# Optimization experiments

Hardware: AMD Instinct MI355X
Metric: run time of the kernel (lower is better)

Reference implementation:

```python
import jax, jax.numpy as jnp
from jax import lax
import numpy as np

V, H, L = 32000, 512, 256   # vocab, hidden_dim, latent_dim
B, TE, TD = 16, 512, 256    # batch, enc max len, dec max len


def setup_inputs() -> dict:
    key = jax.random.key(0)
    ks = jax.random.split(key, 20)
    s = 0.05
    inp = {}
    inp['emb'] = jax.random.normal(ks[0], (V, H), jnp.float32) * s
    # GRU params, PyTorch layout: W_ih [3H_out, D_in], gate order r,z,n
    inp['enc_Wih'] = jax.random.normal(ks[1], (3 * H, H), jnp.float32) * s
    inp['enc_Whh'] = jax.random.normal(ks[2], (3 * H, H), jnp.float32) * s
    inp['enc_bih'] = jnp.zeros((3 * H,), jnp.float32)
    inp['enc_bhh'] = jnp.zeros((3 * H,), jnp.float32)
    inp['dec_Wih'] = jax.random.normal(ks[3], (3 * L, H), jnp.float32) * s
    inp['dec_Whh'] = jax.random.normal(ks[4], (3 * L, L), jnp.float32) * s
    inp['dec_bih'] = jnp.zeros((3 * L,), jnp.float32)
    inp['dec_bhh'] = jnp.zeros((3 * L,), jnp.float32)
    inp['W_mu'] = jax.random.normal(ks[5], (L, 2 * H), jnp.float32) * s
    inp['b_mu'] = jnp.zeros((L,), jnp.float32)
    inp['W_ls'] = jax.random.normal(ks[6], (L, 2 * H), jnp.float32) * s
    inp['b_ls'] = jnp.zeros((L,), jnp.float32)
    inp['W_fc'] = jax.random.normal(ks[7], (V, L), jnp.float32) * s
    inp['b_fc'] = jnp.zeros((V,), jnp.float32)
    inp['noise'] = jax.random.normal(ks[8], (B, L), jnp.float32)  # reparam eps
    inp['enc_ids'] = jax.random.randint(ks[9], (B, TE), 0, V)
    inp['enc_len'] = jax.random.randint(ks[10], (B,), 1, TE + 1)
    inp['dec_ids'] = jax.random.randint(ks[11], (B, TD), 0, V)
    inp['dec_len'] = jax.random.randint(ks[12], (B,), 1, TD + 1)
    return inp


def gru(x, lengths, h0, Wih, Whh, bih, bhh):
    # x: [B,T,D], h0: [B,Hout]. Emulates packed GRU: state frozen and output
    # zeroed past each sample's length (pad_packed_sequence semantics).
    T = x.shape[1]
    Hout = h0.shape[-1]
    xT = jnp.swapaxes(x, 0, 1)                              # [T,B,D]
    valid = jnp.arange(T)[:, None] < lengths[None, :]       # [T,B]

    def step(h, inp):
        x_t, v = inp
        gx = x_t @ Wih.T + bih                              # [B,3Hout]
        gh = h @ Whh.T + bhh
        r = jax.nn.sigmoid(gx[:, :Hout] + gh[:, :Hout])
        z = jax.nn.sigmoid(gx[:, Hout:2 * Hout] + gh[:, Hout:2 * Hout])
        n = jnp.tanh(gx[:, 2 * Hout:] + r * gh[:, 2 * Hout:])
        h_new = (1.0 - z) * n + z * h
        h_keep = jnp.where(v[:, None], h_new, h)
        out = jnp.where(v[:, None], h_new, 0.0)
        return h_keep, out

    h_last, outs = lax.scan(step, h0, (xT, valid))
    return jnp.swapaxes(outs, 0, 1), h_last                 # [B,T,Hout], [B,Hout]


def masked_softmax(scores, mask):
    s = jnp.where(mask, scores, -jnp.inf)
    a = jax.nn.softmax(s, axis=-1)
    return jnp.where(mask, a, 0.0)


def reference(emb, enc_Wih, enc_Whh, enc_bih, enc_bhh,
              dec_Wih, dec_Whh, dec_bih, dec_bhh,
              W_mu, b_mu, W_ls, b_ls, W_fc, b_fc, noise,
              enc_ids, enc_len, dec_ids, dec_len):
    # ---- encode ----
    x_enc = emb[enc_ids]                                    # [B,TE,H]
    h0 = jnp.zeros((x_enc.shape[0], H), x_enc.dtype)
    out, last_state = gru(x_enc, enc_len, h0, enc_Wih, enc_Whh, enc_bih, enc_bhh)
    mask = jnp.arange(out.shape[1])[None, :] < enc_len[:, None]   # [B,TE]
    # batched masked attention pooling (replaces per-sample _return_weight loop)
    first_state = out[:, 0, :]                              # out[0] always valid
    alpha_fw = masked_softmax(jnp.einsum('btd,bd->bt', out, last_state), mask)
    alpha_bw = masked_softmax(jnp.einsum('btd,bd->bt', out, first_state), mask)
    alpha = 0.5 * (alpha_fw + alpha_bw)
    semantic = jnp.einsum('bt,btd->bd', alpha, out)
    h_enc = jnp.concatenate([last_state, semantic], axis=1)  # [B,2H]
    # ---- sample latent ----
    mu = h_enc @ W_mu.T + b_mu
    sigma = jnp.exp(h_enc @ W_ls.T + b_ls)
    z = mu + sigma * noise
    # ---- decode ----
    x_dec = emb[dec_ids]                                    # [B,TD,H]
    dec_out, _ = gru(x_dec, dec_len, z, dec_Wih, dec_Whh, dec_bih, dec_bhh)
    logits = dec_out @ W_fc.T + b_fc                        # [B,TD,V]
    dec_max_len = jnp.max(dec_len)
    return logits, dec_max_len, mu, sigma
```

## Files before the change

### kernel.cpp

```cpp
#include <hip/hip_runtime.h>
#include <hip/hip_bf16.h>
#include <stdint.h>

#define B 16
#define H 512
#define L 256
#define TE 512
#define TD 256
#define NV 32000

typedef __attribute__((ext_vector_type(8))) __bf16 bf16x8;
typedef __attribute__((ext_vector_type(4))) float f32x4;
typedef __attribute__((ext_vector_type(8))) unsigned short u16x8;
typedef __attribute__((ext_vector_type(4))) unsigned short u16x4;
typedef unsigned short u16;
typedef unsigned long long u64;

__device__ __forceinline__ u16 f2bf(float f) {
  unsigned u = __float_as_uint(f);
  u += 0x7fffu + ((u >> 16) & 1u);
  return (u16)(u >> 16);
}
__device__ __forceinline__ float fast_sigmoid(float x) {
  return __builtin_amdgcn_rcpf(1.f + __expf(-x));
}
__device__ __forceinline__ float fast_tanh(float x) {
  float e = __expf(2.f * x);
  return 1.f - 2.f * __builtin_amdgcn_rcpf(e + 1.f);
}

__device__ __forceinline__ u16x8 pack8(float4 a, float4 c) {
  u16x8 r;
  r[0] = f2bf(a.x); r[1] = f2bf(a.y); r[2] = f2bf(a.z); r[3] = f2bf(a.w);
  r[4] = f2bf(c.x); r[5] = f2bf(c.y); r[6] = f2bf(c.z); r[7] = f2bf(c.w);
  return r;
}

__global__ __launch_bounds__(256) void k_f2bf(const float* __restrict__ in,
                                              u16* __restrict__ outp, long n) {
  long i = ((long)blockIdx.x * 256 + threadIdx.x) * 8;
  if (i + 8 > n) return;
  float4 a = *(const float4*)&in[i];
  float4 c = *(const float4*)&in[i + 4];
  *(u16x8*)&outp[i] = pack8(a, c);
}

__global__ __launch_bounds__(256) void k_gather(const float* __restrict__ emb,
                                                const int* __restrict__ ids,
                                                u16* __restrict__ X, int rows) {
  int gid = blockIdx.x * 256 + threadIdx.x;
  int m = gid >> 6, seg = gid & 63;
  if (m >= rows) return;
  long src = (long)ids[m] * H + seg * 8;
  float4 a = *(const float4*)&emb[src];
  float4 c = *(const float4*)&emb[src + 4];
  *(u16x8*)&X[(long)m * H + seg * 8] = pack8(a, c);
}

__global__ __launch_bounds__(256) void k_gemm_bt(const u16* __restrict__ A,
                                                 const u16* __restrict__ Bw,
                                                 const float* __restrict__ bias,
                                                 float* __restrict__ C,
                                                 int M, int N, int K) {
  constexpr int LDSK = 72;
  __shared__ u16 Al[128 * LDSK];
  __shared__ u16 Bl[128 * LDSK];
  const int tid = threadIdx.x;
  const int lane = tid & 63;
  const int wave = tid >> 6;
  const int wr = (wave >> 1) * 64, wc = (wave & 1) * 64;
  const long tM = (long)blockIdx.y * 128, tN = (long)blockIdx.x * 128;
  const int r32 = tid >> 3;
  const int c8 = (tid & 7) * 8;
  const u16* Ag = A + (tM + r32) * (long)K + c8;
  const u16* Bg = Bw + (tN + r32) * (long)K + c8;
  const int fr = lane & 15;
  const int fq = lane >> 4;
  f32x4 acc[4][4] = {};

  for (int kb = 0; kb < K; kb += 64) {
    u16x8 ta0 = *(const u16x8*)(Ag + kb);
    u16x8 ta1 = *(const u16x8*)(Ag + 32 * (long)K + kb);
    u16x8 ta2 = *(const u16x8*)(Ag + 64 * (long)K + kb);
    u16x8 ta3 = *(const u16x8*)(Ag + 96 * (long)K + kb);
    u16x8 tb0 = *(const u16x8*)(Bg + kb);
    u16x8 tb1 = *(const u16x8*)(Bg + 32 * (long)K + kb);
    u16x8 tb2 = *(const u16x8*)(Bg + 64 * (long)K + kb);
    u16x8 tb3 = *(const u16x8*)(Bg + 96 * (long)K + kb);
    __syncthreads();
    *(u16x8*)&Al[(r32 +  0) * LDSK + c8] = ta0;
    *(u16x8*)&Al[(r32 + 32) * LDSK + c8] = ta1;
    *(u16x8*)&Al[(r32 + 64) * LDSK + c8] = ta2;
    *(u16x8*)&Al[(r32 + 96) * LDSK + c8] = ta3;
    *(u16x8*)&Bl[(r32 +  0) * LDSK + c8] = tb0;
    *(u16x8*)&Bl[(r32 + 32) * LDSK + c8] = tb1;
    *(u16x8*)&Bl[(r32 + 64) * LDSK + c8] = tb2;
    *(u16x8*)&Bl[(r32 + 96) * LDSK + c8] = tb3;
    __syncthreads();
#pragma unroll
    for (int ks = 0; ks < 2; ks++) {
      const int kcol = ks * 32 + fq * 8;
      bf16x8 av[4], bv[4];
#pragma unroll
      for (int mi = 0; mi < 4; mi++)
        av[mi] = __builtin_bit_cast(bf16x8, *(const u16x8*)&Al[(wr + mi * 16 + fr) * LDSK + kcol]);
#pragma unroll
      for (int ni = 0; ni < 4; ni++)
        bv[ni] = __builtin_bit_cast(bf16x8, *(const u16x8*)&Bl[(wc + ni * 16 + fr) * LDSK + kcol]);
#pragma unroll
      for (int mi = 0; mi < 4; mi++)
#pragma unroll
        for (int ni = 0; ni < 4; ni++)
          acc[mi][ni] = __builtin_amdgcn_mfma_f32_16x16x32_bf16(av[mi], bv[ni], acc[mi][ni], 0, 0, 0);
    }
  }
#pragma unroll
  for (int mi = 0; mi < 4; mi++) {
    long row = tM + wr + mi * 16 + fq * 4;
#pragma unroll
    for (int ni = 0; ni < 4; ni++) {
      long col = tN + wc + ni * 16 + fr;
      float bs = bias[col];
#pragma unroll
      for (int r = 0; r < 4; r++)
        C[(row + r) * (long)N + col] = acc[mi][ni][r] + bs;
    }
  }
}

template <bool ENC, int HD, int T, int UPW>
__global__ __launch_bounds__(256) void k_gru7(const float* __restrict__ GX,
                                              const float* __restrict__ Whh,
                                              const float* __restrict__ bhh,
                                              const int* __restrict__ lens,
                                              u64* __restrict__ Hbuf,
                                              const float* __restrict__ h0f,
                                              float* __restrict__ out_f32,
                                              u16* __restrict__ out_bf,
                                              float* __restrict__ hlast) {
  constexpr int G2 = UPW / 16;
  constexpr int ROWS = 3 * UPW;
  constexpr int LDH = HD + 8;
  constexpr int WPB = HD / 2;
  constexpr int NWORD = 16 * WPB;
  constexpr int PW = NWORD / 256;
  __shared__ u16 w_lds[ROWS][LDH];
  __shared__ u16 h_lds[16][LDH];

  const int tid = threadIdx.x;
  const int u0 = blockIdx.x * UPW;
  const int lane = tid & 63, wv = tid >> 6;
  const int fr = lane & 15, fq = lane >> 4;
  const bool cw = wv < G2;
  const int u = u0 + wv * 16 + fr;

  for (int i = tid; i < ROWS * HD / 4; i += 256) {
    int rr = i / (HD / 4), c = (i % (HD / 4)) * 4;
    int tt = rr >> 4, fr_ = rr & 15;
    int grow = (tt % 3) * HD + u0 + (tt / 3) * 16 + fr_;
    float4 v = *(const float4*)&Whh[(long)grow * HD + c];
    u16x4 p; p[0] = f2bf(v.x); p[1] = f2bf(v.y); p[2] = f2bf(v.z); p[3] = f2bf(v.w);
    *(u16x4*)&w_lds[rr][c] = p;
  }
  int tmax = 1;
#pragma unroll
  for (int i = 0; i < 16; i++) tmax = max(tmax, lens[i]);

  float bh[3], hold[4];
  int len4[4];
#pragma unroll
  for (int g = 0; g < 3; g++) bh[g] = cw ? bhh[g * HD + u] : 0.f;
#pragma unroll
  for (int r = 0; r < 4; r++) {
    len4[r] = cw ? lens[fq * 4 + r] : 0;
    hold[r] = (ENC || !cw) ? 0.f : h0f[(fq * 4 + r) * HD + u];
  }
  __syncthreads();

  for (int t = 0; ; t++) {
    const u64* Hc = Hbuf + (size_t)(t & 1) * NWORD;
    u64* Hn = Hbuf + (size_t)((t + 1) & 1) * NWORD;
    float gxr[3][4];
    if (cw) {
#pragma unroll
      for (int g = 0; g < 3; g++)
#pragma unroll
        for (int r = 0; r < 4; r++)
          gxr[g][r] = GX[((size_t)(fq * 4 + r) * T + t) * 3 * HD + g * HD + u];
    }
    const unsigned want = (unsigned)t;
    u64 vv[PW];
#pragma unroll
    for (int i = 0; i < PW; i++)
      vv[i] = __hip_atomic_load(&Hc[i * 256 + tid], __ATOMIC_RELAXED, __HIP_MEMORY_SCOPE_AGENT);
    for (;;) {
      bool ok = true;
#pragma unroll
      for (int i = 0; i < PW; i++) ok &= ((unsigned)(vv[i] >> 32) == want);
      if (ok) break;
#pragma unroll
      for (int i = 0; i < PW; i++)
        if ((unsigned)(vv[i] >> 32) != want)
          vv[i] = __hip_atomic_load(&Hc[i * 256 + tid], __ATOMIC_RELAXED, __HIP_MEMORY_SCOPE_AGENT);
    }
#pragma unroll
    for (int i = 0; i < PW; i++) {
      int w = i * 256 + tid;
      *(unsigned*)&h_lds[w / WPB][(w % WPB) * 2] = (unsigned)vv[i];
    }
    __syncthreads();
    if (cw) {
      f32x4 accg[3] = {};
#pragma unroll
      for (int kk = 0; kk < HD / 32; kk++) {
        int kc = kk * 32 + fq * 8;
        bf16x8 av = __builtin_bit_cast(bf16x8, *(const u16x8*)&h_lds[fr][kc]);
#pragma unroll
        for (int g = 0; g < 3; g++) {
          bf16x8 bv = __builtin_bit_cast(bf16x8,
              *(const u16x8*)&w_lds[(wv * 3 + g) * 16 + fr][kc]);
          accg[g] = __builtin_amdgcn_mfma_f32_16x16x32_bf16(av, bv, accg[g], 0, 0, 0);
        }
      }
#pragma unroll
      for (int r = 0; r < 4; r++) {
        const int bb = fq * 4 + r;
        const bool val = t < len4[r];
        float rr_ = fast_sigmoid(accg[0][r] + bh[0] + gxr[0][r]);
        float zz  = fast_sigmoid(accg[1][r] + bh[1] + gxr[1][r]);
        float nn  = fast_tanh(gxr[2][r] + rr_ * (accg[2][r] + bh[2]));
        float hnew = (1.f - zz) * nn + zz * hold[r];
        float hk = val ? hnew : hold[r];
        hold[r] = hk;
        float sh = __shfl_xor(hk, 1);
        if (!(fr & 1)) {
          u64 pw = ((u64)(unsigned)(t + 1) << 32) |
                   ((unsigned)f2bf(sh) << 16) | f2bf(hk);
          __hip_atomic_store(&Hn[(size_t)bb * WPB + ((unsigned)u >> 1)], pw,
                             __ATOMIC_RELAXED, __HIP_MEMORY_SCOPE_AGENT);
          if constexpr (ENC) {
            float2 o = val ? make_float2(hk, sh) : make_float2(0.f, 0.f);
            *(float2*)&out_f32[((size_t)bb * T + t) * HD + u] = o;
          } else {
            unsigned ow = val ? (((unsigned)f2bf(sh) << 16) | f2bf(hk)) : 0u;
            *(unsigned*)&out_bf[((size_t)bb * T + t) * HD + u] = ow;
          }
        }
      }
    }
    __syncthreads();
    if (t + 1 >= tmax) break;
  }

  if (cw) {
    if constexpr (ENC) {
#pragma unroll
      for (int r = 0; r < 4; r++) hlast[(fq * 4 + r) * HD + u] = hold[r];
    }
  }
  if constexpr (ENC) {
    float4 z4 = make_float4(0.f, 0.f, 0.f, 0.f);
    for (int bb = 0; bb < 16; bb++)
      for (int x = tid; x < (T - tmax) * HD / 4; x += 256) {
        int t2 = tmax + (x * 4) / HD, c = (x * 4) % HD;
        *(float4*)&out_f32[((size_t)bb * T + t2) * HD + c] = z4;
      }
  } else {
    u16x8 z8 = {};
    for (int bb = 0; bb < 16; bb++)
      for (int x = tid; x < (T - tmax) * HD / 8; x += 256) {
        int t2 = tmax + (x * 8) / HD, c = (x * 8) % HD;
        *(u16x8*)&out_bf[((size_t)bb * T + t2) * HD + c] = z8;
      }
  }
}

__global__ __launch_bounds__(256) void k_middle(const float* __restrict__ out_enc,
                                                const float* __restrict__ hlast,
                                                const int* __restrict__ enc_len,
                                                const float* __restrict__ W_mu,
                                                const float* __restrict__ b_mu,
                                                const float* __restrict__ W_ls,
                                                const float* __restrict__ b_ls,
                                                const float* __restrict__ noise,
                                                const int* __restrict__ dec_len,
                                                float* __restrict__ out_tail,
                                                float* __restrict__ zf,
                                                u64* __restrict__ hbw) {
  const int b = blockIdx.x, tid = threadIdx.x;
  __shared__ float last[H], first[H], sfw[TE], sbw[TE], alpha[TE], sem[H];
  __shared__ float redA[256], redB[256];
  __shared__ u16 zbf[L];
  const int len = enc_len[b];
  for (int i = tid; i < H; i += 256) {
    last[i] = hlast[b * H + i];
    first[i] = out_enc[((size_t)b * TE) * H + i];
  }
  __syncthreads();
  for (int t = tid; t < TE; t += 256) {
    float afw = 0.f, abw = 0.f;
    if (t < len) {
      const float4* op = (const float4*)&out_enc[((size_t)b * TE + t) * H];
      for (int i = 0; i < H / 4; i++) {
        float4 o = op[i];
        float4 l = *(const float4*)&last[i * 4];
        float4 f = *(const float4*)&first[i * 4];
        afw += o.x * l.x + o.y * l.y + o.z * l.z + o.w * l.w;
        abw += o.x * f.x + o.y * f.y + o.z * f.z + o.w * f.w;
      }
    }
    sfw[t] = afw; sbw[t] = abw;
  }
  __syncthreads();
  float mfw = -3e38f, mbw = -3e38f;
  for (int t = tid; t < len; t += 256) { mfw = fmaxf(mfw, sfw[t]); mbw = fmaxf(mbw, sbw[t]); }
  redA[tid] = mfw; redB[tid] = mbw; __syncthreads();
  for (int s = 128; s > 0; s >>= 1) {
    if (tid < s) { redA[tid] = fmaxf(redA[tid], redA[tid + s]); redB[tid] = fmaxf(redB[tid], redB[tid + s]); }
    __syncthreads();
  }
  const float Mfw = redA[0], Mbw = redB[0];
  __syncthreads();
  float tfw = 0.f, tbw = 0.f;
  for (int t = tid; t < len; t += 256) {
    float e1 = expf(sfw[t] - Mfw); sfw[t] = e1; tfw += e1;
    float e2 = expf(sbw[t] - Mbw); sbw[t] = e2; tbw += e2;
  }
  redA[tid] = tfw; redB[tid] = tbw; __syncthreads();
  for (int s = 128; s > 0; s >>= 1) {
    if (tid < s) { redA[tid] += redA[tid + s]; redB[tid] += redB[tid + s]; }
    __syncthreads();
  }
  const float ifw = 0.5f / redA[0], ibw = 0.5f / redB[0];
  __syncthreads();
  for (int t = tid; t < TE; t += 256) alpha[t] = (t < len) ? (sfw[t] * ifw + sbw[t] * ibw) : 0.f;
  __syncthreads();
  for (int d = tid; d < H; d += 256) {
    float s = 0.f;
    for (int t = 0; t < len; t++) s += alpha[t] * out_enc[((size_t)b * TE + t) * H + d];
    sem[d] = s;
  }
  __syncthreads();
  {
    const int j = tid;
    const float4* wm = (const float4*)&W_mu[(size_t)j * 2 * H];
    const float4* wl = (const float4*)&W_ls[(size_t)j * 2 * H];
    float am = 0.f, al = 0.f;
    for (int i = 0; i < H / 4; i++) {
      float4 hh = *(const float4*)&last[i * 4];
      float4 w1 = wm[i]; am += hh.x * w1.x + hh.y * w1.y + hh.z * w1.z + hh.w * w1.w;
      float4 w2 = wl[i]; al += hh.x * w2.x + hh.y * w2.y + hh.z * w2.z + hh.w * w2.w;
    }
    for (int i = 0; i < H / 4; i++) {
      float4 hh = *(const float4*)&sem[i * 4];
      float4 w1 = wm[H / 4 + i]; am += hh.x * w1.x + hh.y * w1.y + hh.z * w1.z + hh.w * w1.w;
      float4 w2 = wl[H / 4 + i]; al += hh.x * w2.x + hh.y * w2.y + hh.z * w2.z + hh.w * w2.w;
    }
    float muv = am + b_mu[j];
    float sgv = expf(al + b_ls[j]);
    float zv = muv + sgv * noise[b * L + j];
    out_tail[131072001ul + (size_t)b * L + j] = muv;
    out_tail[131076097ul + (size_t)b * L + j] = sgv;
    zf[b * L + j] = zv;
    zbf[j] = f2bf(zv);
  }
  __syncthreads();
  if (tid < L / 2) {
    u64 pw = ((unsigned)zbf[2 * tid + 1] << 16) | (u64)zbf[2 * tid];
    __hip_atomic_store(&hbw[b * (L / 2) + tid], pw,
                       __ATOMIC_RELAXED, __HIP_MEMORY_SCOPE_AGENT);
  }
  if (b == 0 && tid == 0) {
    int m = 0;
    for (int i = 0; i < B; i++) m = max(m, dec_len[i]);
    out_tail[131072000ul] = (float)m;
  }
}

extern "C" void kernel_launch(void* const* d_in, const int* in_sizes, int n_in,
                              void* d_out, int out_size, void* d_ws, size_t ws_size,
                              hipStream_t stream) {
  const float* emb     = (const float*)d_in[0];
  const float* eWih    = (const float*)d_in[1];
  const float* eWhh    = (const float*)d_in[2];
  const float* ebih    = (const float*)d_in[3];
  const float* ebhh    = (const float*)d_in[4];
  const float* dWih    = (const float*)d_in[5];
  const float* dWhh    = (const float*)d_in[6];
  const float* dbih    = (const float*)d_in[7];
  const float* dbhh    = (const float*)d_in[8];
  const float* W_mu    = (const float*)d_in[9];
  const float* b_mu    = (const float*)d_in[10];
  const float* W_ls    = (const float*)d_in[11];
  const float* b_ls    = (const float*)d_in[12];
  const float* W_fc    = (const float*)d_in[13];
  const float* b_fc    = (const float*)d_in[14];
  const float* noise   = (const float*)d_in[15];
  const int*   enc_ids = (const int*)d_in[16];
  const int*   enc_len = (const int*)d_in[17];
  const int*   dec_ids = (const int*)d_in[18];
  const int*   dec_len = (const int*)d_in[19];
  float* out = (float*)d_out;
  char* ws = (char*)d_ws;

  u16*   eWih_bf  = (u16*)(ws + 0);
  u16*   dWih_bf  = (u16*)(ws + 1572864);
  u16*   Wfc_bf   = (u16*)(ws + 2359296);
  u64*   Hbuf_enc = (u64*)(ws + 18743296);
  float* hlast    = (float*)(ws + 18808832);
  u64*   Hbuf_dec = (u64*)(ws + 18841600);
  u16*   dec_out  = (u16*)(ws + 18874368);
  float* zf       = (float*)(ws + 20971520);

  char* ob = (char*)d_out;
  u16*   Xenc_bf = (u16*)(ob + 0);
  u16*   Xdec_bf = (u16*)(ob + 8388608);
  float* GXE     = (float*)(ob + 12582912);
  float* GXD     = (float*)(ob + 62914560);
  float* out_enc = (float*)(ob + 75497472);

  hipMemsetAsync(Hbuf_enc, 0, 65536, stream);
  hipMemsetAsync(Hbuf_dec, 0, 32768, stream);

  k_f2bf<<<384, 256, 0, stream>>>(eWih, eWih_bf, 786432);
  k_f2bf<<<192, 256, 0, stream>>>(dWih, dWih_bf, 393216);
  k_f2bf<<<4000, 256, 0, stream>>>(W_fc, Wfc_bf, 8192000);
  k_gather<<<2048, 256, 0, stream>>>(emb, enc_ids, Xenc_bf, B * TE);
  k_gather<<<1024, 256, 0, stream>>>(emb, dec_ids, Xdec_bf, B * TD);

  k_gemm_bt<<<dim3(12, 64), 256, 0, stream>>>(Xenc_bf, eWih_bf, ebih, GXE, B * TE, 3 * H, H);
  k_gemm_bt<<<dim3(6, 32), 256, 0, stream>>>(Xdec_bf, dWih_bf, dbih, GXD, B * TD, 3 * L, H);

  k_gru7<true, H, TE, 32><<<16, 256, 0, stream>>>(GXE, eWhh, ebhh, enc_len, Hbuf_enc,
                                                  nullptr, out_enc, nullptr, hlast);

  k_middle<<<B, 256, 0, stream>>>(out_enc, hlast, enc_len, W_mu, b_mu, W_ls, b_ls,
                                  noise, dec_len, out, zf, Hbuf_dec);

  k_gru7<false, L, TD, 64><<<4, 256, 0, stream>>>(GXD, dWhh, dbhh, dec_len, Hbuf_dec,
                                                  zf, nullptr, dec_out, nullptr);

  k_gemm_bt<<<dim3(250, 32), 256, 0, stream>>>(dec_out, Wfc_bf, b_fc, out, B * TD, NV, L);
}
```

Before: 2.411 ms.

## Specialize GRU warps: compute waves poll state, helper waves prefetch GX and write outputs

The recurrent GRU kernel now splits each block into two compute waves that spin on the shared hidden state and run the MFMA step, plus two helper waves. The helper waves prefetch the next timestep's input-gate activations into double-buffered LDS and write the previous step's outputs from LDS with coalesced vector stores. This takes global GX loads and scattered output stores off the serial critical path. The decoder now uses 32 units per block with 8 blocks instead of 64 units with 4, which spreads the recurrence over more CUs but means more blocks polling each step.

```diff
diff --git a/kernel.cpp b/kernel.cpp
--- a/kernel.cpp
+++ b/kernel.cpp
@@ -128,8 +128,8 @@
   }
 }
 
-template <bool ENC, int HD, int T, int UPW>
-__global__ __launch_bounds__(256) void k_gru7(const float* __restrict__ GX,
+template <bool ENC, int HD, int T>
+__global__ __launch_bounds__(256) void k_gru8(const float* __restrict__ GX,
                                               const float* __restrict__ Whh,
                                               const float* __restrict__ bhh,
                                               const int* __restrict__ lens,
@@ -138,20 +138,23 @@
                                               float* __restrict__ out_f32,
                                               u16* __restrict__ out_bf,
                                               float* __restrict__ hlast) {
-  constexpr int G2 = UPW / 16;
+  constexpr int UPW = 32;
   constexpr int ROWS = 3 * UPW;
   constexpr int LDH = HD + 8;
   constexpr int WPB = HD / 2;
   constexpr int NWORD = 16 * WPB;
-  constexpr int PW = NWORD / 256;
+  constexpr int PW = NWORD / 128;
   __shared__ u16 w_lds[ROWS][LDH];
   __shared__ u16 h_lds[16][LDH];
+  __shared__ float gx_lds[2][3][16][33];
+  __shared__ float out_lds[2][16][33];
 
   const int tid = threadIdx.x;
   const int u0 = blockIdx.x * UPW;
   const int lane = tid & 63, wv = tid >> 6;
   const int fr = lane & 15, fq = lane >> 4;
-  const bool cw = wv < G2;
+  const bool cw = wv < 2;
+  const int ct = tid & 127;
   const int u = u0 + wv * 16 + fr;
 
   for (int i = tid; i < ROWS * HD / 4; i += 256) {
@@ -175,38 +178,67 @@
     len4[r] = cw ? lens[fq * 4 + r] : 0;
     hold[r] = (ENC || !cw) ? 0.f : h0f[(fq * 4 + r) * HD + u];
   }
+  if (!cw) {
+    const int b = ct >> 3, c0 = (ct & 7) * 4;
+#pragma unroll
+    for (int g = 0; g < 3; g++) {
+      float4 v = *(const float4*)&GX[((size_t)b * T) * 3 * HD + g * HD + u0 + c0];
+      gx_lds[0][g][b][c0 + 0] = v.x; gx_lds[0][g][b][c0 + 1] = v.y;
+      gx_lds[0][g][b][c0 + 2] = v.z; gx_lds[0][g][b][c0 + 3] = v.w;
+    }
+  }
   __syncthreads();
 
   for (int t = 0; ; t++) {
-    const u64* Hc = Hbuf + (size_t)(t & 1) * NWORD;
-    u64* Hn = Hbuf + (size_t)((t + 1) & 1) * NWORD;
-    float gxr[3][4];
+    const int cb_ = t & 1, nb_ = (t + 1) & 1;
     if (cw) {
-#pragma unroll
-      for (int g = 0; g < 3; g++)
-#pragma unroll
-        for (int r = 0; r < 4; r++)
-          gxr[g][r] = GX[((size_t)(fq * 4 + r) * T + t) * 3 * HD + g * HD + u];
-    }
-    const unsigned want = (unsigned)t;
-    u64 vv[PW];
-#pragma unroll
-    for (int i = 0; i < PW; i++)
-      vv[i] = __hip_atomic_load(&Hc[i * 256 + tid], __ATOMIC_RELAXED, __HIP_MEMORY_SCOPE_AGENT);
-    for (;;) {
-      bool ok = true;
-#pragma unroll
-      for (int i = 0; i < PW; i++) ok &= ((unsigned)(vv[i] >> 32) == want);
-      if (ok) break;
+      const u64* Hc = Hbuf + (size_t)cb_ * NWORD;
+      const unsigned want = (unsigned)t;
+      u64 vv[PW];
 #pragma unroll
       for (int i = 0; i < PW; i++)
-        if ((unsigned)(vv[i] >> 32) != want)
-          vv[i] = __hip_atomic_load(&Hc[i * 256 + tid], __ATOMIC_RELAXED, __HIP_MEMORY_SCOPE_AGENT);
-    }
-#pragma unroll
-    for (int i = 0; i < PW; i++) {
-      int w = i * 256 + tid;
-      *(unsigned*)&h_lds[w / WPB][(w % WPB) * 2] = (unsigned)vv[i];
+        vv[i] = __hip_atomic_load(&Hc[i * 128 + ct], __ATOMIC_RELAXED, __HIP_MEMORY_SCOPE_AGENT);
+      for (;;) {
+        bool ok = true;
+#pragma unroll
+        for (int i = 0; i < PW; i++) ok &= ((unsigned)(vv[i] >> 32) == want);
+        if (ok) break;
+#pragma unroll
+        for (int i = 0; i < PW; i++)
+          if ((unsigned)(vv[i] >> 32) != want)
+            vv[i] = __hip_atomic_load(&Hc[i * 128 + ct], __ATOMIC_RELAXED, __HIP_MEMORY_SCOPE_AGENT);
+      }
+#pragma unroll
+      for (int i = 0; i < PW; i++) {
+        int w = i * 128 + ct;
+        *(unsigned*)&h_lds[w / WPB][(w % WPB) * 2] = (unsigned)vv[i];
+      }
+    } else {
+      const int b = ct >> 3;
+      if (t > 0) {
+        const int pb = (t - 1) & 1;
+        const float* ol = &out_lds[pb][b][0];
+        if constexpr (ENC) {
+          const int c0 = (ct & 7) * 4;
+          float4 o = make_float4(ol[c0], ol[c0 + 1], ol[c0 + 2], ol[c0 + 3]);
+          *(float4*)&out_f32[((size_t)b * T + (t - 1)) * HD + u0 + c0] = o;
+        } else {
+          const int w0 = (ct & 7) * 4;
+          uint2 o;
+          o.x = ((unsigned)f2bf(ol[w0 + 1]) << 16) | f2bf(ol[w0]);
+          o.y = ((unsigned)f2bf(ol[w0 + 3]) << 16) | f2bf(ol[w0 + 2]);
+          *(uint2*)&out_bf[((size_t)b * T + (t - 1)) * HD + u0 + w0] = o;
+        }
+      }
+      if (t + 1 < tmax) {
+        const int c0 = (ct & 7) * 4;
+#pragma unroll
+        for (int g = 0; g < 3; g++) {
+          float4 v = *(const float4*)&GX[((size_t)b * T + t + 1) * 3 * HD + g * HD + u0 + c0];
+          gx_lds[nb_][g][b][c0 + 0] = v.x; gx_lds[nb_][g][b][c0 + 1] = v.y;
+          gx_lds[nb_][g][b][c0 + 2] = v.z; gx_lds[nb_][g][b][c0 + 3] = v.w;
+        }
+      }
     }
     __syncthreads();
     if (cw) {
@@ -222,29 +254,25 @@
           accg[g] = __builtin_amdgcn_mfma_f32_16x16x32_bf16(av, bv, accg[g], 0, 0, 0);
         }
       }
+      u64* Hn = Hbuf + (size_t)nb_ * NWORD;
 #pragma unroll
       for (int r = 0; r < 4; r++) {
         const int bb = fq * 4 + r;
         const bool val = t < len4[r];
-        float rr_ = fast_sigmoid(accg[0][r] + bh[0] + gxr[0][r]);
-        float zz  = fast_sigmoid(accg[1][r] + bh[1] + gxr[1][r]);
-        float nn  = fast_tanh(gxr[2][r] + rr_ * (accg[2][r] + bh[2]));
+        const int uc = wv * 16 + fr;
+        float rr_ = fast_sigmoid(accg[0][r] + bh[0] + gx_lds[cb_][0][bb][uc]);
+        float zz  = fast_sigmoid(accg[1][r] + bh[1] + gx_lds[cb_][1][bb][uc]);
+        float nn  = fast_tanh(gx_lds[cb_][2][bb][uc] + rr_ * (accg[2][r] + bh[2]));
         float hnew = (1.f - zz) * nn + zz * hold[r];
         float hk = val ? hnew : hold[r];
         hold[r] = hk;
+        out_lds[cb_][bb][uc] = val ? hnew : 0.f;
         float sh = __shfl_xor(hk, 1);
         if (!(fr & 1)) {
           u64 pw = ((u64)(unsigned)(t + 1) << 32) |
                    ((unsigned)f2bf(sh) << 16) | f2bf(hk);
           __hip_atomic_store(&Hn[(size_t)bb * WPB + ((unsigned)u >> 1)], pw,
                              __ATOMIC_RELAXED, __HIP_MEMORY_SCOPE_AGENT);
-          if constexpr (ENC) {
-            float2 o = val ? make_float2(hk, sh) : make_float2(0.f, 0.f);
-            *(float2*)&out_f32[((size_t)bb * T + t) * HD + u] = o;
-          } else {
-            unsigned ow = val ? (((unsigned)f2bf(sh) << 16) | f2bf(hk)) : 0u;
-            *(unsigned*)&out_bf[((size_t)bb * T + t) * HD + u] = ow;
-          }
         }
       }
     }
@@ -256,6 +284,21 @@
     if constexpr (ENC) {
 #pragma unroll
       for (int r = 0; r < 4; r++) hlast[(fq * 4 + r) * HD + u] = hold[r];
+    }
+  } else {
+    const int b = ct >> 3;
+    const int pb = (tmax - 1) & 1;
+    const float* ol = &out_lds[pb][b][0];
+    if constexpr (ENC) {
+      const int c0 = (ct & 7) * 4;
+      float4 o = make_float4(ol[c0], ol[c0 + 1], ol[c0 + 2], ol[c0 + 3]);
+      *(float4*)&out_f32[((size_t)b * T + (tmax - 1)) * HD + u0 + c0] = o;
+    } else {
+      const int w0 = (ct & 7) * 4;
+      uint2 o;
+      o.x = ((unsigned)f2bf(ol[w0 + 1]) << 16) | f2bf(ol[w0]);
+      o.y = ((unsigned)f2bf(ol[w0 + 3]) << 16) | f2bf(ol[w0 + 2]);
+      *(uint2*)&out_bf[((size_t)b * T + (tmax - 1)) * HD + u0 + w0] = o;
     }
   }
   if constexpr (ENC) {
@@ -431,14 +474,14 @@
   k_gemm_bt<<<dim3(12, 64), 256, 0, stream>>>(Xenc_bf, eWih_bf, ebih, GXE, B * TE, 3 * H, H);
   k_gemm_bt<<<dim3(6, 32), 256, 0, stream>>>(Xdec_bf, dWih_bf, dbih, GXD, B * TD, 3 * L, H);
 
-  k_gru7<true, H, TE, 32><<<16, 256, 0, stream>>>(GXE, eWhh, ebhh, enc_len, Hbuf_enc,
-                                                  nullptr, out_enc, nullptr, hlast);
+  k_gru8<true, H, TE><<<16, 256, 0, stream>>>(GXE, eWhh, ebhh, enc_len, Hbuf_enc,
+                                              nullptr, out_enc, nullptr, hlast);
 
   k_middle<<<B, 256, 0, stream>>>(out_enc, hlast, enc_len, W_mu, b_mu, W_ls, b_ls,
                                   noise, dec_len, out, zf, Hbuf_dec);
 
-  k_gru7<false, L, TD, 64><<<4, 256, 0, stream>>>(GXD, dWhh, dbhh, dec_len, Hbuf_dec,
-                                                  zf, nullptr, dec_out, nullptr);
+  k_gru8<false, L, TD><<<8, 256, 0, stream>>>(GXD, dWhh, dbhh, dec_len, Hbuf_dec,
+                                              zf, nullptr, dec_out, nullptr);
 
   k_gemm_bt<<<dim3(250, 32), 256, 0, stream>>>(dec_out, Wfc_bf, b_fc, out, B * TD, NV, L);
 }
```

Measured after the change: 2.967 ms. 1.23x slower.
